# Performance work log

Hardware: AMD Instinct MI355X
Metric: run time of the kernel (lower is better)

## Reference

```python
import jax, jax.numpy as jnp
import numpy as np

NUM_EMBEDDINGS = 1024
EMBEDDING_DIM = 64


def setup_inputs() -> dict:
    key = jax.random.key(0)
    k1, k2 = jax.random.split(key)
    z = jax.random.normal(k1, (64, 32, 32, EMBEDDING_DIM), dtype=jnp.float32)
    # torch init: uniform_(-1/num_embeddings, 1/num_embeddings)
    lim = 1.0 / NUM_EMBEDDINGS
    codebook = jax.random.uniform(
        k2, (NUM_EMBEDDINGS, EMBEDDING_DIM), dtype=jnp.float32,
        minval=-lim, maxval=lim)
    return {"z": z, "codebook": codebook}


def reference(z, codebook):
    # z: [..., D]; codebook: [K, D]
    z_flat = z.reshape(-1, z.shape[-1])                      # [N, D]
    # ||z||^2 - 2 z.e + ||e||^2  -> [N, K]
    distances = (
        jnp.sum(z_flat ** 2, axis=1, keepdims=True)
        - 2.0 * jnp.einsum("nd,kd->nk", z_flat, codebook)
        + jnp.sum(codebook ** 2, axis=1)
    )
    min_indices = jnp.argmin(distances, axis=1)              # [N]
    z_q = jnp.take(codebook, min_indices, axis=0).reshape(z.shape)
    return z_q, min_indices
```

## Files before the change

kernel.cpp:

```cpp
#include <hip/hip_runtime.h>
#include <hip/hip_bf16.h>
#include <math.h>


#define D      64
#define K      1024
#define BR     128
#define BLOCK  256

typedef _Float16 half8_t __attribute__((ext_vector_type(8)));
typedef float    floatx4 __attribute__((ext_vector_type(4)));
typedef unsigned long long u64;

#define WS_KEYS_OFF  0
#define WS_CN_OFF    524288
#define WS_EF_OFF    528384

__device__ __forceinline__ float np_sumsq64_p(const float* __restrict__ x) {
    float r[8];
    {
        float4 v0 = *(const float4*)(x);
        float4 v1 = *(const float4*)(x + 4);
        r[0] = __fmul_rn(v0.x, v0.x); r[1] = __fmul_rn(v0.y, v0.y);
        r[2] = __fmul_rn(v0.z, v0.z); r[3] = __fmul_rn(v0.w, v0.w);
        r[4] = __fmul_rn(v1.x, v1.x); r[5] = __fmul_rn(v1.y, v1.y);
        r[6] = __fmul_rn(v1.z, v1.z); r[7] = __fmul_rn(v1.w, v1.w);
    }
#pragma unroll
    for (int i = 8; i < 64; i += 8) {
        float4 v0 = *(const float4*)(x + i);
        float4 v1 = *(const float4*)(x + i + 4);
        r[0] = __fadd_rn(r[0], __fmul_rn(v0.x, v0.x));
        r[1] = __fadd_rn(r[1], __fmul_rn(v0.y, v0.y));
        r[2] = __fadd_rn(r[2], __fmul_rn(v0.z, v0.z));
        r[3] = __fadd_rn(r[3], __fmul_rn(v0.w, v0.w));
        r[4] = __fadd_rn(r[4], __fmul_rn(v1.x, v1.x));
        r[5] = __fadd_rn(r[5], __fmul_rn(v1.y, v1.y));
        r[6] = __fadd_rn(r[6], __fmul_rn(v1.z, v1.z));
        r[7] = __fadd_rn(r[7], __fmul_rn(v1.w, v1.w));
    }
    return __fadd_rn(__fadd_rn(__fadd_rn(r[0], r[1]), __fadd_rn(r[2], r[3])),
                     __fadd_rn(__fadd_rn(r[4], r[5]), __fadd_rn(r[6], r[7])));
}

__global__ void vq_pre(const float* __restrict__ cb, float* __restrict__ cn,
                       _Float16* __restrict__ ef) {
    const int k = blockIdx.x * 64 + threadIdx.x;
    if (k >= K) return;
    cn[k] = np_sumsq64_p(cb + (long)k * D);
    const int t = k >> 6, ct = (k >> 4) & 3, l16 = k & 15;
#pragma unroll
    for (int ch = 0; ch < 2; ++ch)
#pragma unroll
        for (int quad = 0; quad < 4; ++quad) {
            const float* p = cb + (long)k * D + ch * 32 + quad * 8;
            half8_t h1, h2;
#pragma unroll
            for (int j = 0; j < 8; ++j) {
                float x10 = __fmul_rn(p[j], 1024.0f);
                _Float16 g1 = (_Float16)x10;
                h1[j] = g1;
                h2[j] = (_Float16)(__fmul_rn(__fsub_rn(x10, (float)g1), 2048.0f));
            }
            const int base = t * 8192 + 128 * quad + 8 * l16;
            *(half8_t*)(ef + base + 512 * (ch * 4 + ct))       = h1;
            *(half8_t*)(ef + base + 512 * ((2 + ch) * 4 + ct)) = h2;
        }
}

__global__ __launch_bounds__(BLOCK, 3) void vq_main(
    const float* __restrict__ z, const _Float16* __restrict__ ef,
    const float* __restrict__ cn, u64* __restrict__ keys) {
    __shared__ __align__(16) float zf[BR * 68];
    __shared__ float sS[BR];
    __shared__ float sCn[512];

    const int tid  = threadIdx.x;
    const int lane = tid & 63;
    const int wv   = tid >> 6;
    const int quad = lane >> 4;
    const int l16  = lane & 15;
    const int rb = blockIdx.x >> 1, ks = blockIdx.x & 1;
    const long rowbase = (long)rb * BR;
    const int kb0 = ks * 512;

    const float4* gz = (const float4*)(z + rowbase * D);
#pragma unroll
    for (int i = 0; i < 8; ++i) {
        int idx4 = i * BLOCK + tid;
        int r = idx4 >> 4, j = idx4 & 15;
        *(float4*)(zf + r * 68 + j * 4) = gz[idx4];
    }
    sCn[tid]       = cn[kb0 + tid];
    sCn[tid + 256] = cn[kb0 + tid + 256];
    __syncthreads();

    if (tid < BR) sS[tid] = np_sumsq64_p(zf + tid * 68);

    half8_t a1[2][2], a2[2][2];
#pragma unroll
    for (int rt = 0; rt < 2; ++rt) {
        const int row = wv * 32 + rt * 16 + l16;
#pragma unroll
        for (int ch = 0; ch < 2; ++ch) {
            const float* p = zf + row * 68 + ch * 32 + quad * 8;
            float4 f0 = *(const float4*)(p);
            float4 f1 = *(const float4*)(p + 4);
            float xs[8] = {f0.x, f0.y, f0.z, f0.w, f1.x, f1.y, f1.z, f1.w};
#pragma unroll
            for (int j = 0; j < 8; ++j) {
                _Float16 h1 = (_Float16)xs[j];
                a1[rt][ch][j] = h1;
                a2[rt][ch][j] =
                    (_Float16)(__fmul_rn(__fsub_rn(xs[j], (float)h1), 2048.0f));
            }
        }
    }
    __syncthreads();

    float myS[2][4];
#pragma unroll
    for (int rt = 0; rt < 2; ++rt)
#pragma unroll
        for (int r = 0; r < 4; ++r)
            myS[rt][r] = sS[wv * 32 + rt * 16 + quad * 4 + r];

    float bv[2][4];
    int   bi[2][4];
#pragma unroll
    for (int rt = 0; rt < 2; ++rt)
#pragma unroll
        for (int r = 0; r < 4; ++r) { bv[rt][r] = INFINITY; bi[rt][r] = 0; }

    const _Float16* eb = ef + (long)ks * 8 * 8192;

    for (int t = 0; t < 8; ++t) {
        const _Float16* tb = eb + t * 8192 + 8 * lane;
        const int kbase = kb0 + t * 64;
#pragma unroll
        for (int ctp = 0; ctp < 2; ++ctp) {
            half8_t b1[2][2], b2[2][2];
#pragma unroll
            for (int ct2 = 0; ct2 < 2; ++ct2) {
                const int ct = ctp * 2 + ct2;
#pragma unroll
                for (int ch = 0; ch < 2; ++ch) {
                    b1[ct2][ch] = *(const half8_t*)(tb + 512 * (ch * 4 + ct));
                    b2[ct2][ch] = *(const half8_t*)(tb + 512 * ((2 + ch) * 4 + ct));
                }
            }
#pragma unroll
            for (int rt = 0; rt < 2; ++rt) {
                floatx4 aM[2], aC[2];
#pragma unroll
                for (int c = 0; c < 2; ++c) {
                    aM[c] = (floatx4){0.f, 0.f, 0.f, 0.f};
                    aC[c] = (floatx4){0.f, 0.f, 0.f, 0.f};
                }
#pragma unroll
                for (int ch = 0; ch < 2; ++ch)
#pragma unroll
                    for (int c = 0; c < 2; ++c) {
                        aM[c] = __builtin_amdgcn_mfma_f32_16x16x32_f16(
                            a1[rt][ch], b1[c][ch], aM[c], 0, 0, 0);
                        aC[c] = __builtin_amdgcn_mfma_f32_16x16x32_f16(
                            a1[rt][ch], b2[c][ch], aC[c], 0, 0, 0);
                        aC[c] = __builtin_amdgcn_mfma_f32_16x16x32_f16(
                            a2[rt][ch], b1[c][ch], aC[c], 0, 0, 0);
                    }
#pragma unroll
                for (int c = 0; c < 2; ++c) {
                    const int ct = ctp * 2 + c;
                    const float cnv = sCn[t * 64 + ct * 16 + l16];
                    const int kg = kbase + ct * 16 + l16;
#pragma unroll
                    for (int r = 0; r < 4; ++r) {
                        float ds = fmaf(aC[c][r], 0x1p-11f, aM[c][r]);
                        float t2 = __fmul_rn(ds, 0x1p-9f);
                        float dist = __fadd_rn(__fsub_rn(myS[rt][r], t2), cnv);
                        if (dist < bv[rt][r]) { bv[rt][r] = dist; bi[rt][r] = kg; }
                    }
                }
            }
        }
    }

#pragma unroll
    for (int rt = 0; rt < 2; ++rt)
#pragma unroll
        for (int r = 0; r < 4; ++r) {
            float v = bv[rt][r];
            int   x = bi[rt][r];
#pragma unroll
            for (int off = 1; off <= 8; off <<= 1) {
                float ov = __shfl_xor(v, off);
                int   ox = __shfl_xor(x, off);
                if (ov < v || (ov == v && ox < x)) { v = ov; x = ox; }
            }
            if (l16 == 0) {
                const long row = rowbase + wv * 32 + rt * 16 + quad * 4 + r;
                u64 key = ((u64)__float_as_uint(v) << 32) | (unsigned)x;
                atomicMin(&keys[row], key);
            }
        }
}

__global__ void vq_resolve(const float* __restrict__ cb,
                           const u64* __restrict__ keys,
                           float* __restrict__ zq, float* __restrict__ idx_out) {
    const int gid = blockIdx.x * BLOCK + threadIdx.x;
    const int row = gid >> 4, j = gid & 15;
    const unsigned k = (unsigned)(keys[row] & 0xFFFFFFFFu);
    ((float4*)zq)[gid] = ((const float4*)cb)[(long)k * 16 + j];
    if (j == 0) idx_out[row] = (float)k;
}

extern "C" void kernel_launch(void* const* d_in, const int* in_sizes, int n_in,
                              void* d_out, int out_size, void* d_ws, size_t ws_size,
                              hipStream_t stream) {
    const float* z  = (const float*)d_in[0];
    const float* cb = (const float*)d_in[1];

    const int n_rows = in_sizes[0] / D;
    float* zq      = (float*)d_out;
    float* idx_out = zq + (long)n_rows * D;

    u64*      ws_keys = (u64*)((char*)d_ws + WS_KEYS_OFF);
    float*    ws_cn   = (float*)((char*)d_ws + WS_CN_OFF);
    _Float16* ws_ef   = (_Float16*)((char*)d_ws + WS_EF_OFF);

    hipMemsetAsync(ws_keys, 0xFF, (size_t)n_rows * sizeof(u64), stream);
    vq_pre<<<K / 64, 64, 0, stream>>>(cb, ws_cn, ws_ef);
    vq_main<<<(n_rows / BR) * 2, BLOCK, 0, stream>>>(z, ws_ef, ws_cn, ws_keys);
    vq_resolve<<<(n_rows * 16) / BLOCK, BLOCK, 0, stream>>>(cb, ws_keys, zq, idx_out);
}
```

Baseline: 113.0 us.

## Use single-wave 64-row blocks with four row tiles per wave

Shrinks the main kernel block to one wavefront covering 64 rows, with each wave handling four 16-row tiles instead of two. Each codebook fragment loaded from global memory is now reused across four row tiles, halving B-operand loads per MFMA. The cost is more registers per wave (launch bound drops to 2) and twice as many blocks, each reloading the 512-entry norm slice into shared memory. The resolve kernel keeps its 256-thread launch.

```diff
diff --git a/kernel.cpp b/kernel.cpp
--- a/kernel.cpp
+++ b/kernel.cpp
@@ -5,8 +5,8 @@
 
 #define D      64
 #define K      1024
-#define BR     128
-#define BLOCK  256
+#define BR     64
+#define BLOCK  64
 
 typedef _Float16 half8_t __attribute__((ext_vector_type(8)));
 typedef float    floatx4 __attribute__((ext_vector_type(4)));
@@ -68,16 +68,14 @@
         }
 }
 
-__global__ __launch_bounds__(BLOCK, 3) void vq_main(
+__global__ __launch_bounds__(BLOCK, 2) void vq_main(
     const float* __restrict__ z, const _Float16* __restrict__ ef,
     const float* __restrict__ cn, u64* __restrict__ keys) {
     __shared__ __align__(16) float zf[BR * 68];
     __shared__ float sS[BR];
     __shared__ float sCn[512];
 
-    const int tid  = threadIdx.x;
-    const int lane = tid & 63;
-    const int wv   = tid >> 6;
+    const int lane = threadIdx.x;
     const int quad = lane >> 4;
     const int l16  = lane & 15;
     const int rb = blockIdx.x >> 1, ks = blockIdx.x & 1;
@@ -86,21 +84,21 @@
 
     const float4* gz = (const float4*)(z + rowbase * D);
 #pragma unroll
-    for (int i = 0; i < 8; ++i) {
-        int idx4 = i * BLOCK + tid;
+    for (int i = 0; i < 16; ++i) {
+        int idx4 = i * BLOCK + lane;
         int r = idx4 >> 4, j = idx4 & 15;
         *(float4*)(zf + r * 68 + j * 4) = gz[idx4];
     }
-    sCn[tid]       = cn[kb0 + tid];
-    sCn[tid + 256] = cn[kb0 + tid + 256];
+#pragma unroll
+    for (int i = 0; i < 8; ++i) sCn[i * 64 + lane] = cn[kb0 + i * 64 + lane];
     __syncthreads();
 
-    if (tid < BR) sS[tid] = np_sumsq64_p(zf + tid * 68);
-
-    half8_t a1[2][2], a2[2][2];
-#pragma unroll
-    for (int rt = 0; rt < 2; ++rt) {
-        const int row = wv * 32 + rt * 16 + l16;
+    sS[lane] = np_sumsq64_p(zf + lane * 68);
+
+    half8_t a1[4][2], a2[4][2];
+#pragma unroll
+    for (int rt = 0; rt < 4; ++rt) {
+        const int row = rt * 16 + l16;
 #pragma unroll
         for (int ch = 0; ch < 2; ++ch) {
             const float* p = zf + row * 68 + ch * 32 + quad * 8;
@@ -118,17 +116,17 @@
     }
     __syncthreads();
 
-    float myS[2][4];
-#pragma unroll
-    for (int rt = 0; rt < 2; ++rt)
+    float myS[4][4];
+#pragma unroll
+    for (int rt = 0; rt < 4; ++rt)
 #pragma unroll
         for (int r = 0; r < 4; ++r)
-            myS[rt][r] = sS[wv * 32 + rt * 16 + quad * 4 + r];
-
-    float bv[2][4];
-    int   bi[2][4];
-#pragma unroll
-    for (int rt = 0; rt < 2; ++rt)
+            myS[rt][r] = sS[rt * 16 + quad * 4 + r];
+
+    float bv[4][4];
+    int   bi[4][4];
+#pragma unroll
+    for (int rt = 0; rt < 4; ++rt)
 #pragma unroll
         for (int r = 0; r < 4; ++r) { bv[rt][r] = INFINITY; bi[rt][r] = 0; }
 
@@ -138,55 +136,38 @@
         const _Float16* tb = eb + t * 8192 + 8 * lane;
         const int kbase = kb0 + t * 64;
 #pragma unroll
-        for (int ctp = 0; ctp < 2; ++ctp) {
-            half8_t b1[2][2], b2[2][2];
-#pragma unroll
-            for (int ct2 = 0; ct2 < 2; ++ct2) {
-                const int ct = ctp * 2 + ct2;
-#pragma unroll
-                for (int ch = 0; ch < 2; ++ch) {
-                    b1[ct2][ch] = *(const half8_t*)(tb + 512 * (ch * 4 + ct));
-                    b2[ct2][ch] = *(const half8_t*)(tb + 512 * ((2 + ch) * 4 + ct));
+        for (int ct = 0; ct < 4; ++ct) {
+            half8_t b1[2], b2[2];
+#pragma unroll
+            for (int ch = 0; ch < 2; ++ch) {
+                b1[ch] = *(const half8_t*)(tb + 512 * (ch * 4 + ct));
+                b2[ch] = *(const half8_t*)(tb + 512 * ((2 + ch) * 4 + ct));
+            }
+            const float cnv = sCn[t * 64 + ct * 16 + l16];
+            const int kg = kbase + ct * 16 + l16;
+#pragma unroll
+            for (int rt = 0; rt < 4; ++rt) {
+                floatx4 aM = (floatx4){0.f, 0.f, 0.f, 0.f};
+                floatx4 aC = (floatx4){0.f, 0.f, 0.f, 0.f};
+                aM = __builtin_amdgcn_mfma_f32_16x16x32_f16(a1[rt][0], b1[0], aM, 0, 0, 0);
+                aM = __builtin_amdgcn_mfma_f32_16x16x32_f16(a1[rt][1], b1[1], aM, 0, 0, 0);
+                aC = __builtin_amdgcn_mfma_f32_16x16x32_f16(a1[rt][0], b2[0], aC, 0, 0, 0);
+                aC = __builtin_amdgcn_mfma_f32_16x16x32_f16(a1[rt][1], b2[1], aC, 0, 0, 0);
+                aC = __builtin_amdgcn_mfma_f32_16x16x32_f16(a2[rt][0], b1[0], aC, 0, 0, 0);
+                aC = __builtin_amdgcn_mfma_f32_16x16x32_f16(a2[rt][1], b1[1], aC, 0, 0, 0);
+#pragma unroll
+                for (int r = 0; r < 4; ++r) {
+                    float ds = fmaf(aC[r], 0x1p-11f, aM[r]);
+                    float t2 = __fmul_rn(ds, 0x1p-9f);
+                    float dist = __fadd_rn(__fsub_rn(myS[rt][r], t2), cnv);
+                    if (dist < bv[rt][r]) { bv[rt][r] = dist; bi[rt][r] = kg; }
                 }
             }
-#pragma unroll
-            for (int rt = 0; rt < 2; ++rt) {
-                floatx4 aM[2], aC[2];
-#pragma unroll
-                for (int c = 0; c < 2; ++c) {
-                    aM[c] = (floatx4){0.f, 0.f, 0.f, 0.f};
-                    aC[c] = (floatx4){0.f, 0.f, 0.f, 0.f};
-                }
-#pragma unroll
-                for (int ch = 0; ch < 2; ++ch)
-#pragma unroll
-                    for (int c = 0; c < 2; ++c) {
-                        aM[c] = __builtin_amdgcn_mfma_f32_16x16x32_f16(
-                            a1[rt][ch], b1[c][ch], aM[c], 0, 0, 0);
-                        aC[c] = __builtin_amdgcn_mfma_f32_16x16x32_f16(
-                            a1[rt][ch], b2[c][ch], aC[c], 0, 0, 0);
-                        aC[c] = __builtin_amdgcn_mfma_f32_16x16x32_f16(
-                            a2[rt][ch], b1[c][ch], aC[c], 0, 0, 0);
-                    }
-#pragma unroll
-                for (int c = 0; c < 2; ++c) {
-                    const int ct = ctp * 2 + c;
-                    const float cnv = sCn[t * 64 + ct * 16 + l16];
-                    const int kg = kbase + ct * 16 + l16;
-#pragma unroll
-                    for (int r = 0; r < 4; ++r) {
-                        float ds = fmaf(aC[c][r], 0x1p-11f, aM[c][r]);
-                        float t2 = __fmul_rn(ds, 0x1p-9f);
-                        float dist = __fadd_rn(__fsub_rn(myS[rt][r], t2), cnv);
-                        if (dist < bv[rt][r]) { bv[rt][r] = dist; bi[rt][r] = kg; }
-                    }
-                }
-            }
-        }
-    }
-
-#pragma unroll
-    for (int rt = 0; rt < 2; ++rt)
+        }
+    }
+
+#pragma unroll
+    for (int rt = 0; rt < 4; ++rt)
 #pragma unroll
         for (int r = 0; r < 4; ++r) {
             float v = bv[rt][r];
@@ -198,7 +179,7 @@
                 if (ov < v || (ov == v && ox < x)) { v = ov; x = ox; }
             }
             if (l16 == 0) {
-                const long row = rowbase + wv * 32 + rt * 16 + quad * 4 + r;
+                const long row = rowbase + rt * 16 + quad * 4 + r;
                 u64 key = ((u64)__float_as_uint(v) << 32) | (unsigned)x;
                 atomicMin(&keys[row], key);
             }
@@ -208,7 +189,7 @@
 __global__ void vq_resolve(const float* __restrict__ cb,
                            const u64* __restrict__ keys,
                            float* __restrict__ zq, float* __restrict__ idx_out) {
-    const int gid = blockIdx.x * BLOCK + threadIdx.x;
+    const int gid = blockIdx.x * 256 + threadIdx.x;
     const int row = gid >> 4, j = gid & 15;
     const unsigned k = (unsigned)(keys[row] & 0xFFFFFFFFu);
     ((float4*)zq)[gid] = ((const float4*)cb)[(long)k * 16 + j];
@@ -232,5 +213,5 @@
     hipMemsetAsync(ws_keys, 0xFF, (size_t)n_rows * sizeof(u64), stream);
     vq_pre<<<K / 64, 64, 0, stream>>>(cb, ws_cn, ws_ef);
     vq_main<<<(n_rows / BR) * 2, BLOCK, 0, stream>>>(z, ws_ef, ws_cn, ws_keys);
-    vq_resolve<<<(n_rows * 16) / BLOCK, BLOCK, 0, stream>>>(cb, ws_keys, zq, idx_out);
-}
+    vq_resolve<<<(n_rows * 16) / 256, 256, 0, stream>>>(cb, ws_keys, zq, idx_out);
+}
```

Result: no change. 111.5 us (-1.3%).
